# Performance work log

Hardware: AMD Instinct MI355X
Metric: run time of the kernel (lower is better)

## Reference

```python
import jax, jax.numpy as jnp
import numpy as np
import math

LAYERS = 30
LAYERS_PER_STACK = 10  # layers // stacks
SCALES = [4, 4, 4, 4]  # total upsampling 256
SQRT_HALF = math.sqrt(0.5)


def _dilated_conv1d(x, w, b, dilation):
    # x: (B, Cin, T), w: (Cout, Cin, K), non-causal SAME padding
    p = (w.shape[-1] - 1) // 2 * dilation
    y = jax.lax.conv_general_dilated(
        x, w, window_strides=(1,), padding=[(p, p)],
        rhs_dilation=(dilation,), dimension_numbers=('NCH', 'OIH', 'NCH'))
    return y + b[None, :, None]


def _conv1x1(x, w):
    # x: (B, Cin, T), w: (Cout, Cin)
    return jnp.einsum('oc,bct->bot', w, x)


def _upsample(c, W_cin, W_up):
    # ConvInUpsampleNetwork with aux_context_window=0: 1x1 conv_in (no bias)
    c = _conv1x1(c, W_cin)                      # (B, 80, T')
    u = c[:, None]                              # (B, 1, 80, T')
    for i, s in enumerate(SCALES):
        u = jnp.repeat(u, s, axis=-1)           # Stretch2d nearest along time
        u = jax.lax.conv_general_dilated(
            u, W_up[i], window_strides=(1, 1), padding=[(0, 0), (s, s)],
            dimension_numbers=('NCHW', 'OIHW', 'NCHW'))  # kernel (1, 2s+1), no bias
    return u[:, 0]                              # (B, 80, T)


def setup_inputs() -> dict:
    key = jax.random.key(0)
    ks = jax.random.split(key, 20)
    B, T_frames, T = 2, 128, 32768
    rc, gc, sc, ac = 64, 128, 64, 80
    sd = 0.05
    inp = {
        'x': jax.random.normal(ks[0], (B, 1, T), jnp.float32),
        'c': jax.random.normal(ks[1], (B, ac, T_frames), jnp.float32),
        'W_first': jax.random.normal(ks[2], (rc, 1), jnp.float32) * sd,
        'b_first': jnp.zeros((rc,), jnp.float32),
        'W_cin': jax.random.normal(ks[3], (ac, ac), jnp.float32) * sd,
        'W_up': jax.random.normal(ks[4], (len(SCALES), 1, 1, 1, 9), jnp.float32) * 0.1
                + 1.0 / 9.0,  # near averaging-filter init
        'Wd': jax.random.normal(ks[5], (LAYERS, gc, rc, 3), jnp.float32) * sd,
        'bd': jnp.zeros((LAYERS, gc), jnp.float32),
        'Wa': jax.random.normal(ks[6], (LAYERS, gc, ac), jnp.float32) * sd,
        'Ws': jax.random.normal(ks[7], (LAYERS, sc, gc // 2), jnp.float32) * sd,
        'bs': jnp.zeros((LAYERS, sc), jnp.float32),
        'Wr': jax.random.normal(ks[8], (LAYERS, rc, gc // 2), jnp.float32) * sd,
        'br': jnp.zeros((LAYERS, rc), jnp.float32),
        'Wl1': jax.random.normal(ks[9], (sc, sc), jnp.float32) * sd,
        'bl1': jnp.zeros((sc,), jnp.float32),
        'Wl2': jax.random.normal(ks[10], (1, sc), jnp.float32) * sd,
        'bl2': jnp.zeros((1,), jnp.float32),
    }
    return inp


def reference(x, c, W_first, b_first, W_cin, W_up, Wd, bd, Wa, Ws, bs, Wr, br,
              Wl1, bl1, Wl2, bl2):
    # upsample conditioning to sample rate
    c_up = _upsample(c, W_cin, W_up)            # (B, 80, T)
    # first 1x1 conv
    h = _conv1x1(x, W_first) + b_first[None, :, None]  # (B, 64, T)
    skips = jnp.zeros_like(_conv1x1(h, Ws[0]))  # (B, 64, T) placeholder shape
    skips = 0.0
    for i in range(LAYERS):
        d = 2 ** (i % LAYERS_PER_STACK)
        g = _dilated_conv1d(h, Wd[i], bd[i], d)            # (B, 128, T)
        g = g + _conv1x1(c_up, Wa[i])                      # aux conditioning
        xa, xb = jnp.split(g, 2, axis=1)
        z = jnp.tanh(xa) * jax.nn.sigmoid(xb)              # (B, 64, T)
        skips = skips + _conv1x1(z, Ws[i]) + bs[i][None, :, None]
        h = (_conv1x1(z, Wr[i]) + br[i][None, :, None] + h) * SQRT_HALF
    skips = skips * math.sqrt(1.0 / LAYERS)
    y = jax.nn.relu(skips)
    y = _conv1x1(y, Wl1) + bl1[None, :, None]
    y = jax.nn.relu(y)
    y = _conv1x1(y, Wl2) + bl2[None, :, None]
    return y  # (B, 1, T)
```

## Files before the change

kernel.cpp:

```cpp
#include <hip/hip_runtime.h>
#include <math.h>

#define T_LEN 32768
#define NLAYERS 30
#define NBLK 512
#define SQRT_HALF 0.70710678118654752f
#define C30 0.18257418583505537f

typedef short short8 __attribute__((ext_vector_type(8)));
typedef short short4v __attribute__((ext_vector_type(4)));
typedef float float4v __attribute__((ext_vector_type(4)));
typedef unsigned short u16;
typedef unsigned long long u64t;
typedef u64t u64x2 __attribute__((ext_vector_type(2)));

__device__ inline u16 rne_bf16(float f){
    unsigned u = __builtin_bit_cast(unsigned, f);
    u += 0x7fffu + ((u >> 16) & 1u);
    return (u16)(u >> 16);
}
__device__ inline float bf16_to_f32(u16 h){
    unsigned u = ((unsigned)h) << 16;
    return __builtin_bit_cast(float, u);
}
__device__ inline void split_bf16(float f, u16& hi, u16& lo){
    hi = rne_bf16(f);
    float r = f - bf16_to_f32(hi);
    lo = rne_bf16(r);
}

__device__ inline u64t ld_sys(const u16* p){
    return __hip_atomic_load((const u64t*)p, __ATOMIC_RELAXED, __HIP_MEMORY_SCOPE_SYSTEM);
}
__device__ inline void st_sys(u16* p, u64t v){
    __hip_atomic_store((u64t*)p, v, __ATOMIC_RELAXED, __HIP_MEMORY_SCOPE_SYSTEM);
}
__device__ inline unsigned ld_sys32(const unsigned* p){
    return __hip_atomic_load(p, __ATOMIC_RELAXED, __HIP_MEMORY_SCOPE_SYSTEM);
}
__device__ inline void st_sys32(unsigned* p, unsigned v){
    __hip_atomic_store(p, v, __ATOMIC_RELAXED, __HIP_MEMORY_SCOPE_SYSTEM);
}
__device__ inline unsigned ld_ag(const unsigned* p){
    return __hip_atomic_load(p, __ATOMIC_RELAXED, __HIP_MEMORY_SCOPE_AGENT);
}
__device__ inline void st_ag(unsigned* p, unsigned v){
    __hip_atomic_store(p, v, __ATOMIC_RELAXED, __HIP_MEMORY_SCOPE_AGENT);
}

__global__ void prep_wmain(const float* __restrict__ Wd, const float* __restrict__ Wa,
                           u16* __restrict__ WA)
{
    int idx = blockIdx.x * 256 + threadIdx.x;
    if (idx >= NLAYERS * 9 * 8 * 64) return;
    int lane = idx & 63;
    int mb = (idx >> 6) & 7;
    int cc = (idx >> 9) % 9;
    int l_ = (idx >> 9) / 9;
    int m = mb * 16 + (lane & 15);
    int kbase = cc * 32 + (lane >> 4) * 8;
    size_t base = ((size_t)(l_ * 9 + cc)) * 4096 + mb * 512 + lane * 8;
#pragma unroll
    for (int j = 0; j < 8; ++j) {
        int k = kbase + j;
        float v = 0.f;
        if (k < 192) {
            int tap = k >> 6, i = k & 63;
            v = Wd[((size_t)(l_ * 128 + m) * 64 + i) * 3 + tap];
        } else if (k < 272) {
            v = Wa[(size_t)(l_ * 128 + m) * 80 + (k - 192)];
        }
        WA[base + j] = rne_bf16(v);
    }
}

__global__ void prep_wsr(const float* __restrict__ Ws, const float* __restrict__ Wr,
                         u16* __restrict__ W2)
{
    int idx = blockIdx.x * 256 + threadIdx.x;
    if (idx >= NLAYERS * 2 * 8 * 64) return;
    int lane = idx & 63;
    int mb = (idx >> 6) & 7;
    int cc = (idx >> 9) & 1;
    int l_ = idx >> 10;
    int m2 = mb * 16 + (lane & 15);
    int kbase = cc * 32 + (lane >> 4) * 8;
    size_t base = ((size_t)(l_ * 2 + cc)) * 4096 + mb * 512 + lane * 8;
#pragma unroll
    for (int j = 0; j < 8; ++j) {
        int k2 = kbase + j;
        float v = (m2 < 64) ? Ws[(size_t)(l_ * 64 + m2) * 64 + k2]
                            : Wr[(size_t)(l_ * 64 + (m2 - 64)) * 64 + k2];
        W2[base + j] = rne_bf16(v);
    }
}

__global__ void cin_kernel(const float* __restrict__ c, const float* __restrict__ Wcin,
                           float* __restrict__ c1)
{
    int idx = blockIdx.x * 256 + threadIdx.x;
    if (idx >= 2 * 128 * 80) return;
    int o = idx % 80;
    int f = (idx / 80) & 127;
    int b = idx / (80 * 128);
    float acc = 0.f;
    for (int ch = 0; ch < 80; ++ch)
        acc = fmaf(Wcin[o * 80 + ch], c[(b * 80 + ch) * 128 + f], acc);
    c1[idx] = acc;
}

__global__ void up_kernel(const float* __restrict__ in, float* __restrict__ out,
                          const float* __restrict__ w9, int Win)
{
    int idx = blockIdx.x * 256 + threadIdx.x;
    int Wout = Win * 4;
    int total = 2 * Wout * 80;
    if (idx >= total) return;
    int a = idx % 80;
    int t = (idx / 80) % Wout;
    int b = idx / (80 * Wout);
    const float* ip = in + (size_t)b * Win * 80 + a;
    float acc = 0.f;
#pragma unroll
    for (int j = 0; j < 9; ++j) {
        int q = t + j - 4;
        if (q >= 0 && q < Wout) acc = fmaf(w9[j], ip[(size_t)(q >> 2) * 80], acc);
    }
    out[idx] = acc;
}

__global__ void upfinal_kernel(const float* __restrict__ u3, const float* __restrict__ w9,
                               u16* __restrict__ cup)
{
    int idx = blockIdx.x * 256 + threadIdx.x;
    if (idx >= 2 * T_LEN * 96) return;
    int a = idx % 96;
    int t = (idx / 96) & (T_LEN - 1);
    int b = idx / (96 * T_LEN);
    float acc = 0.f;
    if (a < 80) {
        const float* ip = u3 + (size_t)b * 8192 * 80 + a;
#pragma unroll
        for (int j = 0; j < 9; ++j) {
            int q = t + j - 4;
            if (q >= 0 && q < T_LEN) acc = fmaf(w9[j], ip[(size_t)(q >> 2) * 80], acc);
        }
    }
    cup[idx] = rne_bf16(acc);
}

__global__ void bar_init(unsigned* bar){
    int i = blockIdx.x * 256 + threadIdx.x;
    for (int e = i; e < 33792; e += 256 * 64) bar[e] = 0u;
}

__global__ __launch_bounds__(512, 4) void wavenet_kernel(
    const float* __restrict__ x, const float* __restrict__ Wf, const float* __restrict__ bf,
    u16* __restrict__ h0, u16* __restrict__ h1,
    u16* __restrict__ m0, u16* __restrict__ m1,
    const u16* __restrict__ cup,
    const u16* __restrict__ WA_all, const u16* __restrict__ W2_all,
    const float* __restrict__ bd_all, const float* __restrict__ bs_all,
    const float* __restrict__ br_all,
    const float* __restrict__ Wl1, const float* __restrict__ bl1,
    const float* __restrict__ Wl2, const float* __restrict__ bl2,
    float* __restrict__ y, unsigned* __restrict__ bar, unsigned* __restrict__ xcdmap)
{
    __shared__ u16 wa_sm[36864];
    const int tid = threadIdx.x;
    const int l  = tid & 63;
    const int w  = tid >> 6;
    const int lr = l & 15;
    const int lg = l >> 4;
    const int bx = blockIdx.x;
    const int g  = ((bx & 7) << 6) | (bx >> 3);
    const int b  = g >> 8;
    const int gt = g & 255;
    const int t0blk = gt * 128;
    const int n0 = t0blk + w * 16;
    char* zb = (char*)wa_sm + w * 4096;

    unsigned* flagP = bar + 1024;
    unsigned* rdP   = bar + 1024 + 16384;

    int dil_cur = 1;

    auto grid_bar = [&](int k){
        __syncthreads();
        if (tid == 0) {
            const unsigned epoch = (unsigned)(k + 1);
            const int grp = bx & 7;
            unsigned* arr  = bar + grp * 32;
            unsigned* root = bar + 8 * 32;
            unsigned* rel  = bar + 9 * 32 + grp * 32;
            unsigned old = __hip_atomic_fetch_add(arr, 1u, __ATOMIC_RELAXED, __HIP_MEMORY_SCOPE_AGENT);
            if (old == epoch * 64u - 1u) {
                unsigned ro = __hip_atomic_fetch_add(root, 1u, __ATOMIC_RELAXED, __HIP_MEMORY_SCOPE_AGENT);
                if (ro == epoch * 8u - 1u) {
#pragma unroll
                    for (int j = 0; j < 8; ++j)
                        __hip_atomic_store(bar + 9 * 32 + j * 32, epoch, __ATOMIC_RELAXED, __HIP_MEMORY_SCOPE_AGENT);
                }
            }
            while (__hip_atomic_load(rel, __ATOMIC_RELAXED, __HIP_MEMORY_SCOPE_AGENT) < epoch)
                __builtin_amdgcn_s_sleep(16);
        }
        __syncthreads();
        asm volatile("buffer_inv" ::: "memory");
    };

    auto wait_nb = [&](const unsigned* fl, unsigned tgt){
        if (tid < 9 && tid != 4) {
            int jt = gt - 4 + tid;
            if (jt >= 0 && jt < 256) {
                const unsigned* fp = fl + (size_t)(b * 256 + jt) * 32;
                while (ld_ag(fp) < tgt) __builtin_amdgcn_s_sleep(4);
            }
        }
        __syncthreads();
    };

    auto wld = [&](const u16* Wg, int c){ return *(const short8*)(Wg + (size_t)c * 4096 + tid * 8); };
    auto wst = [&](int c, short8 v){ *(short8*)((char*)wa_sm + c * 8192 + tid * 16) = v; };

    unsigned myxcd;
    asm volatile("s_getreg_b32 %0, hwreg(HW_REG_XCC_ID)" : "=s"(myxcd));
    if (tid == 0) st_sys32(xcdmap + g, myxcd);
    grid_bar(0);

    unsigned fmask = 0;
    for (int i = 0; i < 11; ++i) {
        int j = gt - 5 + i;
        if (i != 5 && j >= 0 && j < 256) {
            unsigned xv = ld_sys32(xcdmap + b * 256 + j);
            if (xv != myxcd) fmask |= 1u << i;
        }
    }
    int lkT = -1000000, rkT = 1000000;
    for (int i = 4; i >= 0; --i) if ((fmask >> i) & 1) { lkT = t0blk + 128 * (i - 4) - 1; break; }
    for (int i = 6; i <= 10; ++i) if ((fmask >> i) & 1) { rkT = t0blk + 128 * (i - 5); break; }

    u16* hih = h0;
    u16* hoh = h1;
    u16* mih = m0;
    u16* moh = m1;
    const short8 zero8 = (short8)0;

    auto issue_bfrag = [&](int cc, short8& BH){
        if (cc < 6) {
            const int tap = cc >> 1;
            const int i0 = (cc & 1) * 32 + lg * 8;
            const int offd = (tap - 1) * dil_cur;
            int ws0 = n0 + offd;
            int a0 = ws0 < 0 ? 0 : ws0;
            int a1 = (ws0 + 15 >= T_LEN) ? (T_LEN - 1) : (ws0 + 15);
            bool mir = false;
            if (a0 <= a1) {
                int i_0 = (a0 >> 7) - gt + 5;
                int i_1 = (a1 >> 7) - gt + 5;
                mir = ((fmask >> i_0) & 1) || ((fmask >> i_1) & 1);
            }
            int t = n0 + lr + offd;
            if ((unsigned)t < (unsigned)T_LEN) {
                size_t off = ((size_t)b * T_LEN + t) * 64 + i0;
                if (mir) {
                    u64x2 qh;
                    qh.x = ld_sys(mih + off); qh.y = ld_sys(mih + off + 4);
                    BH = __builtin_bit_cast(short8, qh);
                } else {
                    BH = *(const short8*)(hih + off);
                }
            } else { BH = zero8; }
        } else {
            const int a0 = (cc - 6) * 32 + lg * 8;
            int t = n0 + lr;
            BH = *(const short8*)(cup + ((size_t)b * T_LEN + t) * 96 + a0);
        }
    };

#pragma unroll
    for (int e = 0; e < 4; ++e) {
        int q = e * 512 + tid;
        int tl = q >> 4, ch0 = (q & 15) * 4;
        int t = t0blk + tl;
        size_t bt = (size_t)b * T_LEN + t;
        float xv = x[bt];
        short4v hv4;
#pragma unroll
        for (int r = 0; r < 4; ++r) {
            float v = fmaf(Wf[ch0 + r], xv, bf[ch0 + r]);
            hv4[r] = (short)rne_bf16(v);
        }
        *(short4v*)(h0 + bt * 64 + ch0) = hv4;
        if ((t - lkT <= 33) || (rkT - t <= 33))
            st_sys(m0 + bt * 64 + ch0, __builtin_bit_cast(u64t, hv4));
    }

    float4v skipacc[4];
#pragma unroll
    for (int mb = 0; mb < 4; ++mb) skipacc[mb] = (float4v)0.f;

    __syncthreads();
    if (tid == 0) st_ag(flagP + (size_t)g * 32, 1u);

    {
        short8 r0 = wld(WA_all, 0), r1 = wld(WA_all, 1), r2 = wld(WA_all, 2), r3 = wld(WA_all, 3);
        short8 r4 = wld(WA_all, 4), r5 = wld(WA_all, 5), r6 = wld(WA_all, 6),
               r7 = wld(WA_all, 7), r8 = wld(WA_all, 8);
        wst(0, r0); wst(1, r1); wst(2, r2); wst(3, r3);
        wst(4, r4); wst(5, r5); wst(6, r6); wst(7, r7); wst(8, r8);
        __syncthreads();
    }

    for (int l_ = 0; l_ < NLAYERS; ++l_) {
        dil_cur = 1 << (l_ % 10);
        const int dnext = (l_ < NLAYERS - 1) ? (1 << ((l_ + 1) % 10)) : 0;
        const int thr = dnext + 32;
        const u16* WAn = WA_all + (size_t)(l_ + 1) * 9 * 4096;
        const u16* W2 = W2_all + (size_t)l_ * 2 * 4096;
        const float* bd = bd_all + l_ * 128;
        const float* bs = bs_all + l_ * 64;
        const float* br = br_all + l_ * 64;

        wait_nb(flagP, (unsigned)(l_ + 1));
        asm volatile("buffer_inv" ::: "memory");

        float4v acc[8];
#pragma unroll
        for (int mb = 0; mb < 8; ++mb) acc[mb] = (float4v)0.f;

        short8 p0, p1, p2;
        issue_bfrag(0, p0);
        issue_bfrag(1, p1);
        issue_bfrag(2, p2);
#pragma unroll
        for (int cc = 0; cc < 9; ++cc) {
            short8 bh;
            if ((cc % 3) == 0)      { bh = p0; if (cc + 3 < 9) issue_bfrag(cc + 3, p0); }
            else if ((cc % 3) == 1) { bh = p1; if (cc + 3 < 9) issue_bfrag(cc + 3, p1); }
            else                    { bh = p2; if (cc + 3 < 9) issue_bfrag(cc + 3, p2); }
            const char* cbuf = (const char*)wa_sm + cc * 8192;
#pragma unroll
            for (int mb = 0; mb < 8; ++mb) {
                short8 ah = *(const short8*)(cbuf + mb * 1024 + l * 16);
                acc[mb] = __builtin_amdgcn_mfma_f32_16x16x32_bf16(ah, bh, acc[mb], 0, 0, 0);
            }
        }
        __syncthreads();
        if (tid == 0) st_ag(rdP + (size_t)g * 32, (unsigned)(l_ + 1));

        short4v ehq[4];
        {
            int t = n0 + lr;
#pragma unroll
            for (int m = 0; m < 4; ++m) {
                size_t off = ((size_t)b * T_LEN + t) * 64 + m * 16 + lg * 4;
                ehq[m] = *(const short4v*)(hih + off);
            }
        }

#pragma unroll
        for (int mb = 0; mb < 4; ++mb) {
            const float4v bda = *(const float4v*)(bd + mb * 16 + lg * 4);
            const float4v bdb = *(const float4v*)(bd + 64 + mb * 16 + lg * 4);
            int t = lr;
            short4v zhv;
#pragma unroll
            for (int r = 0; r < 4; ++r) {
                float xa = acc[mb][r] + bda[r];
                float xb = acc[mb + 4][r] + bdb[r];
                float e2 = __expf(2.f * xa);
                float th = 1.f - 2.f * __builtin_amdgcn_rcpf(e2 + 1.f);
                float sg = __builtin_amdgcn_rcpf(1.f + __expf(-xb));
                zhv[r] = (short)rne_bf16(th * sg);
            }
            unsigned byteoff = (unsigned)((t * 64 + mb * 16 + lg * 4) * 2) ^ ((unsigned)(t & 7) << 4);
            *(short4v*)(zb + byteoff) = zhv;
        }

        if (l_ != NLAYERS - 1) {
            short8 r4 = wld(WAn, 4), r5 = wld(WAn, 5), r6 = wld(WAn, 6),
                   r7 = wld(WAn, 7), r8 = wld(WAn, 8);
            wst(4, r4); wst(5, r5); wst(6, r6); wst(7, r7); wst(8, r8);
        }

        float4v acc2[8];
#pragma unroll
        for (int mb = 0; mb < 8; ++mb) acc2[mb] = (float4v)0.f;

#pragma unroll
        for (int c2 = 0; c2 < 2; ++c2) {
            int t = lr;
            unsigned k0 = (unsigned)(c2 * 32 + lg * 8);
            unsigned byteoff = (unsigned)((t * 64 + k0) * 2) ^ ((unsigned)(t & 7) << 4);
            short8 b2h = *(const short8*)(zb + byteoff);
#pragma unroll
            for (int mb = 0; mb < 8; ++mb) {
                short8 ah = *(const short8*)(W2 + (size_t)c2 * 4096 + mb * 512 + l * 8);
                acc2[mb] = __builtin_amdgcn_mfma_f32_16x16x32_bf16(ah, b2h, acc2[mb], 0, 0, 0);
            }
        }

        if (l_ != NLAYERS - 1) wait_nb(rdP, (unsigned)l_);

#pragma unroll
        for (int mb = 0; mb < 8; ++mb) {
            int ch0 = (mb & 3) * 16 + lg * 4;
            if (mb < 4) {
                const float4v bsv = *(const float4v*)(bs + ch0);
                skipacc[mb] = skipacc[mb] + acc2[mb] + bsv;
            } else if (l_ != NLAYERS - 1) {
                const float4v brv = *(const float4v*)(br + ch0);
                int t = n0 + lr;
                size_t off = ((size_t)b * T_LEN + t) * 64 + ch0;
                short4v hv = ehq[mb - 4];
                short4v ohv;
#pragma unroll
                for (int r = 0; r < 4; ++r) {
                    float hr = bf16_to_f32((u16)hv[r]);
                    float xo = (acc2[mb][r] + brv[r] + hr) * SQRT_HALF;
                    ohv[r] = (short)rne_bf16(xo);
                }
                *(short4v*)(hoh + off) = ohv;
                if ((t - lkT <= thr) || (rkT - t <= thr))
                    st_sys(moh + off, __builtin_bit_cast(u64t, ohv));
            }
        }

        if (l_ != NLAYERS - 1) {
            __syncthreads();
            if (tid == 0) st_ag(flagP + (size_t)g * 32, (unsigned)(l_ + 2));
            short8 r0 = wld(WAn, 0), r1 = wld(WAn, 1), r2 = wld(WAn, 2), r3 = wld(WAn, 3);
            wst(0, r0); wst(1, r1); wst(2, r2); wst(3, r3);
            __syncthreads();
        }
        u16* t1;
        t1 = hih; hih = hoh; hoh = t1;
        t1 = mih; mih = moh; moh = t1;
    }

    __syncthreads();
    char* sk = (char*)wa_sm;
#pragma unroll
    for (int mb = 0; mb < 4; ++mb) {
        int tloc = w * 16 + lr;
        int ch0 = mb * 16 + lg * 4;
        unsigned off = (unsigned)((tloc * 64 + ch0) * 4) ^ ((unsigned)(tloc & 7) << 5);
        *(float4v*)(sk + off) = skipacc[mb];
    }
    float* w1s = (float*)((char*)wa_sm + 32768);
    for (int e = tid; e < 4096; e += 512) w1s[e] = Wl1[e];
    __syncthreads();
    if (tid < 128) {
        int tloc = tid;
        float s[64];
#pragma unroll
        for (int i4 = 0; i4 < 16; ++i4) {
            unsigned off = (unsigned)((tloc * 64 + i4 * 4) * 4) ^ ((unsigned)(tloc & 7) << 5);
            float4v v = *(const float4v*)(sk + off);
#pragma unroll
            for (int r = 0; r < 4; ++r) s[i4 * 4 + r] = fmaxf(v[r] * C30, 0.f);
        }
        float acc = bl2[0];
        for (int o = 0; o < 64; ++o) {
            float a = bl1[o];
#pragma unroll
            for (int i = 0; i < 64; ++i) a = fmaf(w1s[o * 64 + i], s[i], a);
            acc = fmaf(Wl2[o], fmaxf(a, 0.f), acc);
        }
        y[(size_t)b * T_LEN + t0blk + tloc] = acc;
    }
}

extern "C" void kernel_launch(void* const* d_in, const int* in_sizes, int n_in,
                              void* d_out, int out_size, void* d_ws, size_t ws_size,
                              hipStream_t stream)
{
    const float* x       = (const float*)d_in[0];
    const float* c       = (const float*)d_in[1];
    const float* W_first = (const float*)d_in[2];
    const float* b_first = (const float*)d_in[3];
    const float* W_cin   = (const float*)d_in[4];
    const float* W_up    = (const float*)d_in[5];
    const float* Wd      = (const float*)d_in[6];
    const float* bd      = (const float*)d_in[7];
    const float* Wa      = (const float*)d_in[8];
    const float* Ws      = (const float*)d_in[9];
    const float* bs      = (const float*)d_in[10];
    const float* Wr      = (const float*)d_in[11];
    const float* br      = (const float*)d_in[12];
    const float* Wl1     = (const float*)d_in[13];
    const float* bl1     = (const float*)d_in[14];
    const float* Wl2     = (const float*)d_in[15];
    const float* bl2     = (const float*)d_in[16];

    char* base = (char*)d_ws;
    size_t off = 0;
    auto alloc = [&](size_t bytes) { char* p = base + off; off += (bytes + 255) & ~(size_t)255; return p; };

    const size_t HSZ = (size_t)2 * T_LEN * 64 * 2;
    u16* cup  = (u16*)alloc((size_t)2 * T_LEN * 96 * 2);
    u16* h0   = (u16*)alloc(HSZ);
    u16* h1   = (u16*)alloc(HSZ);
    u16* m0   = (u16*)alloc(HSZ);
    u16* m1   = (u16*)alloc(HSZ);
    unsigned* bar    = (unsigned*)alloc(33792 * 4);
    unsigned* xcdmap = (unsigned*)alloc(4096);
    char* S = alloc(7200000);
    float* c1 = (float*)(S);
    float* u1 = (float*)(S + 81920);
    float* u2 = (float*)(S + 409600);
    float* u3 = (float*)(S + 1720320);
    u16* WA = (u16*)(S);
    u16* W2 = (u16*)(S + 2211840);

    cin_kernel<<<(2 * 128 * 80 + 255) / 256, 256, 0, stream>>>(c, W_cin, c1);
    up_kernel<<<(2 * 512 * 80 + 255) / 256, 256, 0, stream>>>(c1, u1, W_up + 0, 128);
    up_kernel<<<(2 * 2048 * 80 + 255) / 256, 256, 0, stream>>>(u1, u2, W_up + 9, 512);
    up_kernel<<<(2 * 8192 * 80 + 255) / 256, 256, 0, stream>>>(u2, u3, W_up + 18, 2048);
    upfinal_kernel<<<(2 * T_LEN * 96 + 255) / 256, 256, 0, stream>>>(u3, W_up + 27, cup);

    prep_wmain<<<(NLAYERS * 9 * 8 * 64 + 255) / 256, 256, 0, stream>>>(Wd, Wa, WA);
    prep_wsr<<<(NLAYERS * 2 * 8 * 64 + 255) / 256, 256, 0, stream>>>(Ws, Wr, W2);
    bar_init<<<64, 256, 0, stream>>>(bar);

    wavenet_kernel<<<NBLK, 512, 0, stream>>>(
        x, W_first, b_first,
        h0, h1, m0, m1,
        cup, WA, W2,
        bd, bs, br, Wl1, bl1, Wl2, bl2,
        (float*)d_out, bar, xcdmap);
}
```

Before: 536.4 us.

## Split output channels across wave pairs with 1024-thread blocks

Doubles the block to 1024 threads so each 16-timestep tile is handled by two waves, each computing half of the 128 gate channels (and half of the skip/residual outputs). Pre-activation gates are staged through shared memory so each wave can gather the matching tanh/sigmoid halves, which adds an extra barrier and LDS round-trip per layer. The intent is to halve per-wave accumulator registers and MFMA work, raising parallelism per block while keeping the same grid and barrier scheme.

```diff
diff --git a/kernel.cpp b/kernel.cpp
--- a/kernel.cpp
+++ b/kernel.cpp
@@ -154,7 +154,7 @@
     for (int e = i; e < 33792; e += 256 * 64) bar[e] = 0u;
 }
 
-__global__ __launch_bounds__(512, 4) void wavenet_kernel(
+__global__ __launch_bounds__(1024, 8) void wavenet_kernel(
     const float* __restrict__ x, const float* __restrict__ Wf, const float* __restrict__ bf,
     u16* __restrict__ h0, u16* __restrict__ h1,
     u16* __restrict__ m0, u16* __restrict__ m1,
@@ -170,6 +170,8 @@
     const int tid = threadIdx.x;
     const int l  = tid & 63;
     const int w  = tid >> 6;
+    const int chw = w & 1;
+    const int tg  = w >> 1;
     const int lr = l & 15;
     const int lg = l >> 4;
     const int bx = blockIdx.x;
@@ -177,8 +179,8 @@
     const int b  = g >> 8;
     const int gt = g & 255;
     const int t0blk = gt * 128;
-    const int n0 = t0blk + w * 16;
-    char* zb = (char*)wa_sm + w * 4096;
+    const int n0 = t0blk + tg * 16;
+    char* zg = (char*)wa_sm + tg * 4096;
 
     unsigned* flagP = bar + 1024;
     unsigned* rdP   = bar + 1024 + 16384;
@@ -220,8 +222,8 @@
         __syncthreads();
     };
 
-    auto wld = [&](const u16* Wg, int c){ return *(const short8*)(Wg + (size_t)c * 4096 + tid * 8); };
-    auto wst = [&](int c, short8 v){ *(short8*)((char*)wa_sm + c * 8192 + tid * 16) = v; };
+    auto wld = [&](const u16* Wg, int c){ return *(const short4v*)(Wg + (size_t)c * 4096 + tid * 4); };
+    auto wst = [&](int c, short4v v){ *(short4v*)((char*)wa_sm + c * 8192 + tid * 8) = v; };
 
     unsigned myxcd;
     asm volatile("s_getreg_b32 %0, hwreg(HW_REG_XCC_ID)" : "=s"(myxcd));
@@ -279,8 +281,8 @@
     };
 
 #pragma unroll
-    for (int e = 0; e < 4; ++e) {
-        int q = e * 512 + tid;
+    for (int e = 0; e < 2; ++e) {
+        int q = e * 1024 + tid;
         int tl = q >> 4, ch0 = (q & 15) * 4;
         int t = t0blk + tl;
         size_t bt = (size_t)b * T_LEN + t;
@@ -304,9 +306,9 @@
     if (tid == 0) st_ag(flagP + (size_t)g * 32, 1u);
 
     {
-        short8 r0 = wld(WA_all, 0), r1 = wld(WA_all, 1), r2 = wld(WA_all, 2), r3 = wld(WA_all, 3);
-        short8 r4 = wld(WA_all, 4), r5 = wld(WA_all, 5), r6 = wld(WA_all, 6),
-               r7 = wld(WA_all, 7), r8 = wld(WA_all, 8);
+        short4v r0 = wld(WA_all, 0), r1 = wld(WA_all, 1), r2 = wld(WA_all, 2), r3 = wld(WA_all, 3);
+        short4v r4 = wld(WA_all, 4), r5 = wld(WA_all, 5), r6 = wld(WA_all, 6),
+                r7 = wld(WA_all, 7), r8 = wld(WA_all, 8);
         wst(0, r0); wst(1, r1); wst(2, r2); wst(3, r3);
         wst(4, r4); wst(5, r5); wst(6, r6); wst(7, r7); wst(8, r8);
         __syncthreads();
@@ -325,9 +327,9 @@
         wait_nb(flagP, (unsigned)(l_ + 1));
         asm volatile("buffer_inv" ::: "memory");
 
-        float4v acc[8];
-#pragma unroll
-        for (int mb = 0; mb < 8; ++mb) acc[mb] = (float4v)0.f;
+        float4v acc[4];
+#pragma unroll
+        for (int mb = 0; mb < 4; ++mb) acc[mb] = (float4v)0.f;
 
         short8 p0, p1, p2;
         issue_bfrag(0, p0);
@@ -341,8 +343,8 @@
             else                    { bh = p2; if (cc + 3 < 9) issue_bfrag(cc + 3, p2); }
             const char* cbuf = (const char*)wa_sm + cc * 8192;
 #pragma unroll
-            for (int mb = 0; mb < 8; ++mb) {
-                short8 ah = *(const short8*)(cbuf + mb * 1024 + l * 16);
+            for (int mb = 0; mb < 4; ++mb) {
+                short8 ah = *(const short8*)(cbuf + (chw * 4 + mb) * 1024 + l * 16);
                 acc[mb] = __builtin_amdgcn_mfma_f32_16x16x32_bf16(ah, bh, acc[mb], 0, 0, 0);
             }
         }
@@ -350,7 +352,7 @@
         if (tid == 0) st_ag(rdP + (size_t)g * 32, (unsigned)(l_ + 1));
 
         short4v ehq[4];
-        {
+        if (chw) {
             int t = n0 + lr;
 #pragma unroll
             for (int m = 0; m < 4; ++m) {
@@ -361,59 +363,73 @@
 
 #pragma unroll
         for (int mb = 0; mb < 4; ++mb) {
-            const float4v bda = *(const float4v*)(bd + mb * 16 + lg * 4);
-            const float4v bdb = *(const float4v*)(bd + 64 + mb * 16 + lg * 4);
-            int t = lr;
-            short4v zhv;
-#pragma unroll
-            for (int r = 0; r < 4; ++r) {
-                float xa = acc[mb][r] + bda[r];
-                float xb = acc[mb + 4][r] + bdb[r];
+            int ch0 = (chw * 4 + mb) * 16 + lg * 4;
+            const float4v bda = *(const float4v*)(bd + ch0);
+            short4v gv;
+#pragma unroll
+            for (int r = 0; r < 4; ++r)
+                gv[r] = (short)rne_bf16(acc[mb][r] + bda[r]);
+            unsigned byteoff = (unsigned)(lr * 256 + ch0 * 2) ^ ((unsigned)(lr & 15) << 3);
+            *(short4v*)(zg + byteoff) = gv;
+        }
+        __syncthreads();
+
+        short4v r4, r5, r6, r7, r8;
+        if (l_ != NLAYERS - 1) {
+            r4 = wld(WAn, 4); r5 = wld(WAn, 5); r6 = wld(WAn, 6);
+            r7 = wld(WAn, 7); r8 = wld(WAn, 8);
+        }
+
+        short8 b2[2];
+#pragma unroll
+        for (int c2 = 0; c2 < 2; ++c2) {
+#pragma unroll
+            for (int j = 0; j < 8; ++j) {
+                int ch = c2 * 32 + lg * 8 + j;
+                unsigned offA = (unsigned)(lr * 256 + ch * 2) ^ ((unsigned)(lr & 15) << 3);
+                unsigned offB = (unsigned)(lr * 256 + (ch + 64) * 2) ^ ((unsigned)(lr & 15) << 3);
+                float xa = bf16_to_f32(*(const u16*)(zg + offA));
+                float xb = bf16_to_f32(*(const u16*)(zg + offB));
                 float e2 = __expf(2.f * xa);
                 float th = 1.f - 2.f * __builtin_amdgcn_rcpf(e2 + 1.f);
                 float sg = __builtin_amdgcn_rcpf(1.f + __expf(-xb));
-                zhv[r] = (short)rne_bf16(th * sg);
-            }
-            unsigned byteoff = (unsigned)((t * 64 + mb * 16 + lg * 4) * 2) ^ ((unsigned)(t & 7) << 4);
-            *(short4v*)(zb + byteoff) = zhv;
-        }
-
+                b2[c2][j] = (short)rne_bf16(th * sg);
+            }
+        }
         if (l_ != NLAYERS - 1) {
-            short8 r4 = wld(WAn, 4), r5 = wld(WAn, 5), r6 = wld(WAn, 6),
-                   r7 = wld(WAn, 7), r8 = wld(WAn, 8);
             wst(4, r4); wst(5, r5); wst(6, r6); wst(7, r7); wst(8, r8);
         }
 
-        float4v acc2[8];
-#pragma unroll
-        for (int mb = 0; mb < 8; ++mb) acc2[mb] = (float4v)0.f;
+        float4v acc2[4];
+#pragma unroll
+        for (int mb = 0; mb < 4; ++mb) acc2[mb] = (float4v)0.f;
 
 #pragma unroll
         for (int c2 = 0; c2 < 2; ++c2) {
-            int t = lr;
-            unsigned k0 = (unsigned)(c2 * 32 + lg * 8);
-            unsigned byteoff = (unsigned)((t * 64 + k0) * 2) ^ ((unsigned)(t & 7) << 4);
-            short8 b2h = *(const short8*)(zb + byteoff);
-#pragma unroll
-            for (int mb = 0; mb < 8; ++mb) {
-                short8 ah = *(const short8*)(W2 + (size_t)c2 * 4096 + mb * 512 + l * 8);
-                acc2[mb] = __builtin_amdgcn_mfma_f32_16x16x32_bf16(ah, b2h, acc2[mb], 0, 0, 0);
+#pragma unroll
+            for (int mb = 0; mb < 4; ++mb) {
+                short8 ah = *(const short8*)(W2 + (size_t)c2 * 4096 + (chw * 4 + mb) * 512 + l * 8);
+                acc2[mb] = __builtin_amdgcn_mfma_f32_16x16x32_bf16(ah, b2[c2], acc2[mb], 0, 0, 0);
             }
         }
 
         if (l_ != NLAYERS - 1) wait_nb(rdP, (unsigned)l_);
 
-#pragma unroll
-        for (int mb = 0; mb < 8; ++mb) {
-            int ch0 = (mb & 3) * 16 + lg * 4;
-            if (mb < 4) {
+        if (chw == 0) {
+#pragma unroll
+            for (int mb = 0; mb < 4; ++mb) {
+                int ch0 = mb * 16 + lg * 4;
                 const float4v bsv = *(const float4v*)(bs + ch0);
                 skipacc[mb] = skipacc[mb] + acc2[mb] + bsv;
-            } else if (l_ != NLAYERS - 1) {
+            }
+        } else if (l_ != NLAYERS - 1) {
+#pragma unroll
+            for (int mb = 0; mb < 4; ++mb) {
+                int ch0 = mb * 16 + lg * 4;
                 const float4v brv = *(const float4v*)(br + ch0);
                 int t = n0 + lr;
                 size_t off = ((size_t)b * T_LEN + t) * 64 + ch0;
-                short4v hv = ehq[mb - 4];
+                short4v hv = ehq[mb];
                 short4v ohv;
 #pragma unroll
                 for (int r = 0; r < 4; ++r) {
@@ -430,8 +446,8 @@
         if (l_ != NLAYERS - 1) {
             __syncthreads();
             if (tid == 0) st_ag(flagP + (size_t)g * 32, (unsigned)(l_ + 2));
-            short8 r0 = wld(WAn, 0), r1 = wld(WAn, 1), r2 = wld(WAn, 2), r3 = wld(WAn, 3);
-            wst(0, r0); wst(1, r1); wst(2, r2); wst(3, r3);
+            short4v q0 = wld(WAn, 0), q1 = wld(WAn, 1), q2 = wld(WAn, 2), q3 = wld(WAn, 3);
+            wst(0, q0); wst(1, q1); wst(2, q2); wst(3, q3);
             __syncthreads();
         }
         u16* t1;
@@ -441,15 +457,17 @@
 
     __syncthreads();
     char* sk = (char*)wa_sm;
-#pragma unroll
-    for (int mb = 0; mb < 4; ++mb) {
-        int tloc = w * 16 + lr;
-        int ch0 = mb * 16 + lg * 4;
-        unsigned off = (unsigned)((tloc * 64 + ch0) * 4) ^ ((unsigned)(tloc & 7) << 5);
-        *(float4v*)(sk + off) = skipacc[mb];
+    if (chw == 0) {
+#pragma unroll
+        for (int mb = 0; mb < 4; ++mb) {
+            int tloc = tg * 16 + lr;
+            int ch0 = mb * 16 + lg * 4;
+            unsigned off = (unsigned)((tloc * 64 + ch0) * 4) ^ ((unsigned)(tloc & 7) << 5);
+            *(float4v*)(sk + off) = skipacc[mb];
+        }
     }
     float* w1s = (float*)((char*)wa_sm + 32768);
-    for (int e = tid; e < 4096; e += 512) w1s[e] = Wl1[e];
+    for (int e = tid; e < 4096; e += 1024) w1s[e] = Wl1[e];
     __syncthreads();
     if (tid < 128) {
         int tloc = tid;
@@ -524,7 +542,7 @@
     prep_wsr<<<(NLAYERS * 2 * 8 * 64 + 255) / 256, 256, 0, stream>>>(Ws, Wr, W2);
     bar_init<<<64, 256, 0, stream>>>(bar);
 
-    wavenet_kernel<<<NBLK, 512, 0, stream>>>(
+    wavenet_kernel<<<NBLK, 1024, 0, stream>>>(
         x, W_first, b_first,
         h0, h1, m0, m1,
         cup, WA, W2,
```

Measured after the change: 1.269 ms. 137% more time.
